# Performance work log

Hardware: AMD Instinct MI355X
Metric: run time of the kernel (lower is better)

Reference implementation:

```python
import jax, jax.numpy as jnp
import numpy as np

BLOCK_SIZE = 32
BLOCK_COUNTS = 8
N_MAX = 1024  # max seq len across jagged batch (static)
LN_EPS = 1e-5


def _silu(x):
    return x * jax.nn.sigmoid(x)


def setup_inputs() -> dict:
    key = jax.random.key(0)
    ks = jax.random.split(key, 5)
    T, H, D = 3200, 8, 128
    lengths = np.array([1024, 768, 896, 512], dtype=np.int64)
    offsets = np.concatenate([[0], np.cumsum(lengths)]).astype(np.int64)  # [B+1]
    q = jax.random.normal(ks[0], (T, H, D), jnp.float32)
    k = jax.random.normal(ks[1], (T, H, D), jnp.float32)
    v = jax.random.normal(ks[2], (T, H, D), jnp.float32)
    u = jax.random.normal(ks[3], (T, H, D), jnp.float32)
    Wg = jax.random.normal(ks[4], (H, D, 3), jnp.float32) * 0.05
    bg = jnp.zeros((H, 3), jnp.float32)
    return {"q": q, "k": k, "v": v, "u": u, "Wg": Wg, "bg": bg,
            "x_offsets": jnp.asarray(offsets)}


def _to_padded(jag, offsets, lengths, n):
    # jag: [T, H, D] -> [B, n, H, D], zero padded
    pos = jnp.arange(n)
    idx = offsets[:-1, None] + pos[None, :]                # [B, n]
    valid = pos[None, :] < lengths[:, None]                # [B, n]
    g = jag[jnp.clip(idx, 0, jag.shape[0] - 1)]            # [B, n, H, D]
    return jnp.where(valid[..., None, None], g, 0.0)


def _to_jagged(padded, offsets, T):
    tok = jnp.arange(T)
    b = jnp.searchsorted(offsets, tok, side='right') - 1   # batch id per token
    m = tok - offsets[b]                                   # local position
    return padded[b, m]


def _forward(q, k, v, u, Wg, bg, x_offsets):
    T, H, D = q.shape
    B = x_offsets.shape[0] - 1
    n = N_MAX
    bs = BLOCK_SIZE
    nb = n // bs
    S = min(BLOCK_COUNTS, nb)
    scale = D ** (-0.5)
    lengths = x_offsets[1:] - x_offsets[:-1]

    qp = _to_padded(q, x_offsets, lengths, n)  # [B, n, H, D]
    kp = _to_padded(k, x_offsets, lengths, n)
    vp = _to_padded(v, x_offsets, lengths, n)

    # gate model: per-head linear D->3 + sigmoid
    gates = jax.nn.sigmoid(jnp.einsum('bmhd,hde->bmhe', qp, Wg) + bg)
    g_cmp, g_slc = gates[..., 0], gates[..., 1]  # [B, n, H]

    # --- block compression ---
    k_cmp = kp.reshape(B, nb, bs, H, D).mean(axis=2)  # [B, nb, H, D]
    v_cmp = vp.reshape(B, nb, bs, H, D).mean(axis=2)

    # --- compressed attention + top-k block selection ---
    scores = jnp.einsum('bmhd,bkhd->bhmk', qp, k_cmp) * scale  # [B, H, n, nb]
    qblk = jnp.arange(n) // bs
    causal = qblk[:, None] >= jnp.arange(nb)[None, :]          # [n, nb]
    masked_scores = jnp.where(causal[None, None], scores, -jnp.inf)
    _, topk = jax.lax.top_k(masked_scores, S)                  # [B, H, n, S]
    topk = jnp.where(topk > qblk[None, None, :, None], -1, topk)

    p_cmp = jnp.where(causal[None, None], _silu(scores), 0.0)
    o_cmp = jnp.einsum('bhmk,bkhd->bmhd', p_cmp, v_cmp) * g_cmp[..., None]

    # --- selected (gathered top-k block) attention ---
    topk_p = jnp.transpose(topk, (0, 2, 1, 3))                 # [B, n, H, S]
    Kb = kp.reshape(B, nb, bs, H, D).transpose(0, 1, 3, 2, 4)  # [B, nb, H, bs, D]
    Vb = vp.reshape(B, nb, bs, H, D).transpose(0, 1, 3, 2, 4)
    b_ix = jnp.arange(B)[:, None, None]
    h_ix = jnp.arange(H)[None, None, :]
    m_pos = jnp.arange(n)
    off = jnp.arange(bs)

    def body(acc, s_idx):
        blk = jnp.take(topk_p, s_idx, axis=3)                  # [B, n, H]
        blk_c = jnp.maximum(blk, 0)
        Ks = Kb[b_ix, blk_c, h_ix]                             # [B, n, H, bs, D]
        Vs = Vb[b_ix, blk_c, h_ix]
        sc = jnp.einsum('bmhd,bmhkd->bmhk', qp, Ks) * scale    # [B, n, H, bs]
        kpos = blk_c[..., None] * bs + off                     # [B, n, H, bs]
        ok = (blk >= 0)[..., None] & (kpos <= m_pos[None, :, None, None])
        p = jnp.where(ok, _silu(sc), 0.0)
        acc = acc + jnp.einsum('bmhk,bmhkd->bmhd', p, Vs)
        return acc, None

    acc, _ = jax.lax.scan(jax.checkpoint(body), jnp.zeros_like(qp), jnp.arange(S))
    o_slc = acc * g_slc[..., None]

    # back to jagged, LayerNorm over flattened (H*D), gate by u
    o_cmp_j = _to_jagged(o_cmp, x_offsets, T)
    o_slc_j = _to_jagged(o_slc, x_offsets, T)

    def ln_u(x):
        xf = x.reshape(T, H * D)
        mu = xf.mean(-1, keepdims=True)
        var = ((xf - mu) ** 2).mean(-1, keepdims=True)
        xn = (xf - mu) * jax.lax.rsqrt(var + LN_EPS)
        return xn.reshape(T, H, D) * u

    out = ln_u(o_cmp_j) + ln_u(o_slc_j)
    return out, qp, kp


def reference(q, k, v, u, Wg, bg, x_offsets):
    return _forward(q, k, v, u, Wg, bg, x_offsets)
```

## Files before the change

### kernel.cpp

```cpp
#include <hip/hip_runtime.h>
#include <hip/hip_bf16.h>
#include <cmath>

#define H 8
#define D 128
#define HD 1024
#define NMAX 1024
#define BS 32
#define NB 32
#define S_SEL 8
#define CHUNK 8
#define MC 4
#define KP 136
#define NXCD 8
#define SCALE 0.08838834764831845f
#define SENT -3.0e38f

typedef __attribute__((ext_vector_type(8))) short short8;
typedef __attribute__((ext_vector_type(4))) float f32x4;

#define MFMA16(a, b, c) __builtin_amdgcn_mfma_f32_16x16x32_bf16(a, b, c, 0, 0, 0)

__device__ __forceinline__ float silu(float x) {
    return x * __builtin_amdgcn_rcpf(1.f + __expf(-x));
}
__device__ __forceinline__ float sigmoid_fast(float x) {
    return __builtin_amdgcn_rcpf(1.f + __expf(-x));
}
__device__ __forceinline__ unsigned short f2bf(float x) {
    return __builtin_bit_cast(unsigned short, __float2bfloat16(x));
}
__device__ __forceinline__ float bfup(unsigned short b) {
    unsigned u = (unsigned)b << 16;
    return __builtin_bit_cast(float, u);
}
__device__ __forceinline__ void split3(float x, unsigned short& b0,
                                       unsigned short& b1, unsigned short& b2) {
    b0 = f2bf(x);
    float r1 = x - bfup(b0);
    b1 = f2bf(r1);
    float r2 = r1 - bfup(b1);
    b2 = f2bf(r2);
}

__global__ __launch_bounds__(256) void prep_kernel(
    const float* __restrict__ q, const float* __restrict__ k,
    const float* __restrict__ v, const float* __restrict__ Wg,
    const float* __restrict__ bg, const int* __restrict__ offs,
    unsigned short* __restrict__ kb16, unsigned short* __restrict__ vt_blk,
    float* __restrict__ g, unsigned short* __restrict__ kc0,
    unsigned short* __restrict__ kc1, unsigned short* __restrict__ kc2,
    unsigned short* __restrict__ vt_cmp, float* __restrict__ o_slc,
    float* __restrict__ qp, float* __restrict__ kp) {
    int x = blockIdx.x;
    int nt = x & (NB - 1);
    int h = (x >> 5) & 7;
    int b = x >> 8;
    int o0 = offs[b];
    int len = offs[b + 1] - o0;
    int tid = threadIdx.x;
    size_t bh = (size_t)(b * H + h);
    int j = tid >> 3, dc = tid & 7;
    size_t pbase = (size_t)((b * NMAX + nt * BS + j)) * HD + h * D + dc * 16;
    if (nt * BS >= len) {
        if (tid < 128) {
            kc0[(bh * NB + nt) * 128 + tid] = 0;
            kc1[(bh * NB + nt) * 128 + tid] = 0;
            kc2[(bh * NB + nt) * 128 + tid] = 0;
            vt_cmp[(bh * 128 + tid) * NB + nt] = 0;
        }
        if (qp) {
            float4 z = make_float4(0.f, 0.f, 0.f, 0.f);
#pragma unroll
            for (int i = 0; i < 4; i++) {
                *(float4*)(qp + pbase + i * 4) = z;
                *(float4*)(kp + pbase + i * 4) = z;
            }
        }
        return;
    }

    __shared__ __align__(16) unsigned short tile[128 * 40];
    __shared__ float redK[4][128];
    __shared__ float redV[4][128];
    int w = tid >> 6, lane = tid & 63;
    size_t base = (size_t)(o0 + nt * BS + j) * HD + h * D + dc * 16;

    {
        float4 z = make_float4(0.f, 0.f, 0.f, 0.f);
#pragma unroll
        for (int i = 0; i < 4; i++) *(float4*)(o_slc + base + i * 4) = z;
    }

    {
        float xv[16];
        *(float4*)(xv + 0)  = *(const float4*)(k + base);
        *(float4*)(xv + 4)  = *(const float4*)(k + base + 4);
        *(float4*)(xv + 8)  = *(const float4*)(k + base + 8);
        *(float4*)(xv + 12) = *(const float4*)(k + base + 12);
        short8 lo, hi;
#pragma unroll
        for (int i = 0; i < 8; i++) { lo[i] = (short)f2bf(xv[i]); hi[i] = (short)f2bf(xv[8 + i]); }
        *(short8*)(kb16 + base) = lo;
        *(short8*)(kb16 + base + 8) = hi;
        if (kp) {
#pragma unroll
            for (int i = 0; i < 4; i++) *(float4*)(kp + pbase + i * 4) = *(float4*)(xv + i * 4);
        }
#pragma unroll
        for (int i = 0; i < 16; i++) {
            float s = xv[i];
            s += __shfl_xor(s, 8); s += __shfl_xor(s, 16); s += __shfl_xor(s, 32);
            if (lane < 8) redK[w][lane * 16 + i] = s;
        }
    }
    {
        float xv[16];
        *(float4*)(xv + 0)  = *(const float4*)(v + base);
        *(float4*)(xv + 4)  = *(const float4*)(v + base + 4);
        *(float4*)(xv + 8)  = *(const float4*)(v + base + 8);
        *(float4*)(xv + 12) = *(const float4*)(v + base + 12);
#pragma unroll
        for (int i = 0; i < 16; i++) tile[(dc * 16 + i) * 40 + j] = f2bf(xv[i]);
#pragma unroll
        for (int i = 0; i < 16; i++) {
            float s = xv[i];
            s += __shfl_xor(s, 8); s += __shfl_xor(s, 16); s += __shfl_xor(s, 32);
            if (lane < 8) redV[w][lane * 16 + i] = s;
        }
    }
    {
        float xv[16];
        *(float4*)(xv + 0)  = *(const float4*)(q + base);
        *(float4*)(xv + 4)  = *(const float4*)(q + base + 4);
        *(float4*)(xv + 8)  = *(const float4*)(q + base + 8);
        *(float4*)(xv + 12) = *(const float4*)(q + base + 12);
        if (qp) {
#pragma unroll
            for (int i = 0; i < 4; i++) *(float4*)(qp + pbase + i * 4) = *(float4*)(xv + i * 4);
        }
        float p0 = 0.f, p1 = 0.f;
#pragma unroll
        for (int i = 0; i < 16; i++) {
            int wb = (h * D + dc * 16 + i) * 3;
            p0 += xv[i] * Wg[wb + 0];
            p1 += xv[i] * Wg[wb + 1];
        }
#pragma unroll
        for (int off = 4; off > 0; off >>= 1) {
            p0 += __shfl_xor(p0, off);
            p1 += __shfl_xor(p1, off);
        }
        if (dc == 0) {
            float g0 = sigmoid_fast(p0 + bg[h * 3 + 0]);
            float g1 = sigmoid_fast(p1 + bg[h * 3 + 1]);
            float* gp = g + (size_t)((b * NMAX + nt * BS + j) * H + h) * 2;
            gp[0] = g0; gp[1] = g1;
        }
    }
    __syncthreads();
    {
        int d = tid >> 1, hf = tid & 1;
        short8 a = *(const short8*)(tile + d * 40 + hf * 16);
        short8 c = *(const short8*)(tile + d * 40 + hf * 16 + 8);
        size_t ob = ((bh * NB + nt) * 128 + (size_t)d) * 32 + hf * 16;
        *(short8*)(vt_blk + ob) = a;
        *(short8*)(vt_blk + ob + 8) = c;
    }
    if (tid < 128) {
        int d = tid;
        const float inv = 1.f / 32.f;
        float km = (redK[0][d] + redK[1][d] + redK[2][d] + redK[3][d]) * inv;
        float vm = (redV[0][d] + redV[1][d] + redV[2][d] + redV[3][d]) * inv;
        unsigned short e0, e1, e2;
        split3(km, e0, e1, e2);
        kc0[(bh * NB + nt) * 128 + d] = e0;
        kc1[(bh * NB + nt) * 128 + d] = e1;
        kc2[(bh * NB + nt) * 128 + d] = e2;
        vt_cmp[(bh * 128 + d) * NB + nt] = f2bf(vm);
    }
}

__global__ __launch_bounds__(256) void cmp_attn(
    const float* __restrict__ q, const unsigned short* __restrict__ kc0,
    const unsigned short* __restrict__ kc1, const unsigned short* __restrict__ kc2,
    const unsigned short* __restrict__ vt_cmp, const float* __restrict__ g,
    const int* __restrict__ offs, unsigned* __restrict__ ms_g,
    float* __restrict__ o_cmp_j) {
    int x = blockIdx.x;
    int qtile = 15 - (x & 15);
    int h = (x >> 4) & 7;
    int b = x >> 7;
    int o0 = offs[b];
    int len = offs[b + 1] - o0;
    if (qtile * 64 >= len) return;
    size_t bh = (size_t)(b * H + h);
    int qmax = 2 * qtile + 1;

    __shared__ __align__(16) unsigned short pool[3 * 4352 + 5120 + 2560];
    unsigned short* R0 = pool;
    unsigned short* R1 = pool + 4352;
    unsigned short* R2 = pool + 8704;
    unsigned short* R3 = pool + 13056;
    unsigned short* Ps = pool + 18176;

    int tid = threadIdx.x;
    int w = tid >> 6, lane = tid & 63;
    int r = lane & 15, quad = lane >> 4;
    int stg_j = tid >> 3, stg_dc = tid & 7;
    size_t msbase = (bh << 10) + (size_t)qtile * 64;

    if (stg_j <= qmax) {
        size_t src = (bh * NB + stg_j) * 128 + stg_dc * 16;
        int ofs = stg_j * 136 + stg_dc * 16;
        short8 a0 = *(const short8*)(kc0 + src);
        short8 b0 = *(const short8*)(kc0 + src + 8);
        short8 a1 = *(const short8*)(kc1 + src);
        short8 b1 = *(const short8*)(kc1 + src + 8);
        short8 a2 = *(const short8*)(kc2 + src);
        short8 b2 = *(const short8*)(kc2 + src + 8);
        *(short8*)(R0 + ofs) = a0; *(short8*)(R0 + ofs + 8) = b0;
        *(short8*)(R1 + ofs) = a1; *(short8*)(R1 + ofs + 8) = b1;
        *(short8*)(R2 + ofs) = a2; *(short8*)(R2 + ofs + 8) = b2;
    }
    {
        int d = tid >> 1, hf = tid & 1;
        short8 vv = *(const short8*)(vt_cmp + (bh * 128 + d) * NB + hf * 16);
        short8 vw = *(const short8*)(vt_cmp + (bh * 128 + d) * NB + hf * 16 + 8);
        *(short8*)(R3 + d * 40 + hf * 16) = vv;
        *(short8*)(R3 + d * 40 + hf * 16 + 8) = vw;
    }
    __syncthreads();

    short8 qf0[4], qf1[4], qf2[4];
    {
        const float* qrow = q + (size_t)(o0 + qtile * 64 + w * 16 + r) * HD + h * D;
#pragma unroll
        for (int s = 0; s < 4; s++) {
            const float* p0 = qrow + s * 32 + quad * 8;
            float xv[8];
            *(float4*)(xv) = *(const float4*)p0;
            *(float4*)(xv + 4) = *(const float4*)(p0 + 4);
            short8 f0, f1, f2;
#pragma unroll
            for (int i = 0; i < 8; i++) {
                unsigned short e0, e1, e2;
                split3(xv[i], e0, e1, e2);
                f0[i] = (short)e0; f1[i] = (short)e1; f2[i] = (short)e2;
            }
            qf0[s] = f0; qf1[s] = f1; qf2[s] = f2;
        }
    }
    auto qk6 = [&](int krow) {
        f32x4 sv = (f32x4){0.f, 0.f, 0.f, 0.f};
#pragma unroll
        for (int s = 0; s < 4; s++) {
            int ofs = krow * 136 + s * 32 + quad * 8;
            short8 k0 = *(const short8*)(R0 + ofs);
            short8 k1 = *(const short8*)(R1 + ofs);
            short8 k2 = *(const short8*)(R2 + ofs);
            sv = MFMA16(qf1[s], k1, sv);
            sv = MFMA16(qf0[s], k2, sv);
            sv = MFMA16(qf2[s], k0, sv);
            sv = MFMA16(qf0[s], k1, sv);
            sv = MFMA16(qf1[s], k0, sv);
            sv = MFMA16(qf0[s], k0, sv);
        }
        return sv;
    };
    f32x4 s0 = qk6(r);
    f32x4 s1 = (f32x4){0.f, 0.f, 0.f, 0.f};
    if (qtile >= 8) s1 = qk6(16 + r);

    float v0[4], v1[4];
#pragma unroll
    for (int jf = 0; jf < 2; jf++) {
        f32x4 svv = jf ? s1 : s0;
        int colj = jf * 16 + r;
#pragma unroll
        for (int i = 0; i < 4; i++) {
            int mrow = w * 16 + quad * 4 + i;
            int qb = 2 * qtile + (mrow >> 5);
            bool causal = (colj <= qb);
            float sc = svv[i] * SCALE;
            float val = causal ? sc : SENT;
            if (jf) v1[i] = val; else v0[i] = val;
            Ps[mrow * 40 + colj] = f2bf(causal ? silu(sc) : 0.f);
        }
    }
    if (qtile < 4) {
        if (tid < 64)
            ms_g[msbase + tid] = (1u << (2 * qtile + (tid >> 5) + 1)) - 1u;
    } else {
#pragma unroll
        for (int i = 0; i < 4; i++) {
            float a = v0[i], bb = v1[i];
            int cnt0 = (bb > a) ? 1 : 0;
            int cnt1 = (a >= bb) ? 1 : 0;
#pragma unroll
            for (int m = 1; m < 16; m++) {
                float pa = __shfl_xor(a, m);
                float pb = __shfl_xor(bb, m);
                int pc = r ^ m;
                cnt0 += ((pa > a) || (pa == a && pc < r)) ? 1 : 0;
                cnt0 += (pb > a) ? 1 : 0;
                cnt1 += ((pa > bb) || (pa == bb)) ? 1 : 0;
                cnt1 += ((pb > bb) || (pb == bb && pc < r)) ? 1 : 0;
            }
            bool sel0 = (cnt0 < S_SEL) && (a > -2.9e38f);
            bool sel1 = (cnt1 < S_SEL) && (bb > -2.9e38f);
            unsigned long long bal0 = __ballot(sel0);
            unsigned long long bal1 = __ballot(sel1);
            unsigned mask = (unsigned)((bal0 >> (16 * quad)) & 0xFFFFull)
                          | ((unsigned)((bal1 >> (16 * quad)) & 0xFFFFull) << 16);
            if (r == 0) ms_g[msbase + w * 16 + quad * 4 + i] = mask;
        }
    }
    f32x4 acc[8];
#pragma unroll
    for (int a = 0; a < 8; a++) acc[a] = (f32x4){0.f, 0.f, 0.f, 0.f};
    {
        short8 pf8 = *(const short8*)(Ps + (w * 16 + r) * 40 + quad * 8);
#pragma unroll
        for (int nf = 0; nf < 8; nf++) {
            short8 vf = *(const short8*)(R3 + (nf * 16 + r) * 40 + quad * 8);
            acc[nf] = MFMA16(pf8, vf, acc[nf]);
        }
    }
#pragma unroll
    for (int i = 0; i < 4; i++) {
        int mrow = w * 16 + quad * 4 + i;
        int gm = qtile * 64 + mrow;
        float gc = g[(size_t)((b * NMAX + gm) * H + h) * 2];
        float* dst = o_cmp_j + (size_t)(o0 + gm) * HD + h * D;
#pragma unroll
        for (int nf = 0; nf < 8; nf++)
            dst[nf * 16 + r] = acc[nf][i] * gc;
    }
}

__global__ __launch_bounds__(256) void slc_attn(
    const float* __restrict__ q, const unsigned short* __restrict__ kb16,
    const unsigned short* __restrict__ vt_blk, const float* __restrict__ g,
    const int* __restrict__ offs, const unsigned* __restrict__ ms_g,
    float* __restrict__ o_slc_j) {
    int x = blockIdx.x;
    int xcd = x & (NXCD - 1);
    int rest = x >> 3;
    int group = rest >> 6;
    int inner = rest & 63;
    int bh = group * NXCD + xcd;
    int b = bh >> 3, h = bh & 7;
    int chunk = inner & (MC - 1);
    int mtile = 15 - (inner >> 2);
    int o0 = offs[b];
    int len = offs[b + 1] - o0;
    if (mtile * 64 >= len) return;
    int qmax = 2 * mtile + 1;
    int kb0 = chunk * CHUNK;
    if (kb0 > qmax) return;
    int kend = min(qmax, kb0 + CHUNK - 1);

    __shared__ __align__(16) unsigned short pool[2 * 32 * KP + 2 * 5120 + 2560];
    __shared__ unsigned Ms[64];
    unsigned short* Kst0 = pool;
    unsigned short* Kst1 = pool + 32 * KP;
    unsigned short* Vst0 = pool + 2 * 32 * KP;
    unsigned short* Vst1 = pool + 2 * 32 * KP + 5120;
    unsigned short* Ps   = pool + 2 * 32 * KP + 10240;

    int tid = threadIdx.x;
    int w = tid >> 6, lane = tid & 63;
    int r = lane & 15, quad = lane >> 4;
    int stg_j = tid >> 3, stg_dc = tid & 7;

    if (tid < 64)
        Ms[tid] = ms_g[((size_t)bh << 10) + mtile * 64 + tid];

    short8 qs[4];
    {
        const float* qrow = q + (size_t)(o0 + mtile * 64 + w * 16 + r) * HD + h * D;
#pragma unroll
        for (int s = 0; s < 4; s++) {
            const float* p0 = qrow + s * 32 + quad * 8;
            float xv[8];
            *(float4*)(xv) = *(const float4*)p0;
            *(float4*)(xv + 4) = *(const float4*)(p0 + 4);
            short8 f;
#pragma unroll
            for (int i = 0; i < 8; i++) f[i] = (short)f2bf(xv[i]);
            qs[s] = f;
        }
    }
    f32x4 acc[8];
#pragma unroll
    for (int a = 0; a < 8; a++) acc[a] = (f32x4){0.f, 0.f, 0.f, 0.f};

    size_t vtbase = (size_t)(bh * NB) * 4096;
    int vd = tid >> 1, vhf = tid & 1;

    {
        const unsigned short* ks = kb16 + (size_t)(o0 + kb0 * BS + stg_j) * HD + h * D + stg_dc * 16;
        short8 k0 = *(const short8*)ks;
        short8 k1 = *(const short8*)(ks + 8);
        *(short8*)(Kst0 + stg_j * KP + stg_dc * 16) = k0;
        *(short8*)(Kst0 + stg_j * KP + stg_dc * 16 + 8) = k1;
        const unsigned short* vs = vt_blk + vtbase + (size_t)kb0 * 4096 + tid * 16;
        short8 v0 = *(const short8*)vs;
        short8 v1 = *(const short8*)(vs + 8);
        *(short8*)(Vst0 + vd * 40 + vhf * 16) = v0;
        *(short8*)(Vst0 + vd * 40 + vhf * 16 + 8) = v1;
    }
    __syncthreads();

    int c = 0;
    for (int kb = kb0; kb <= kend; kb++) {
        short8 pk0, pk1, pv0, pv1;
        bool pf = (kb < kend);
        if (pf) {
            const unsigned short* ks = kb16 + (size_t)(o0 + (kb + 1) * BS + stg_j) * HD + h * D + stg_dc * 16;
            pk0 = *(const short8*)ks;
            pk1 = *(const short8*)(ks + 8);
            const unsigned short* vs = vt_blk + vtbase + (size_t)(kb + 1) * 4096 + tid * 16;
            pv0 = *(const short8*)vs;
            pv1 = *(const short8*)(vs + 8);
        }
        unsigned short* K = c ? Kst1 : Kst0;
        unsigned short* V = c ? Vst1 : Vst0;
        f32x4 s0 = (f32x4){0.f, 0.f, 0.f, 0.f};
        f32x4 s1 = (f32x4){0.f, 0.f, 0.f, 0.f};
#pragma unroll
        for (int s = 0; s < 4; s++) {
            short8 kf0 = *(const short8*)(K + r * KP + s * 32 + quad * 8);
            short8 kf1 = *(const short8*)(K + (16 + r) * KP + s * 32 + quad * 8);
            s0 = MFMA16(qs[s], kf0, s0);
            s1 = MFMA16(qs[s], kf1, s1);
        }
#pragma unroll
        for (int jf = 0; jf < 2; jf++) {
            f32x4 svv = jf ? s1 : s0;
            int colj = jf * 16 + r;
            int kpos = kb * BS + colj;
#pragma unroll
            for (int i = 0; i < 4; i++) {
                int mrow = w * 16 + quad * 4 + i;
                int mpos = mtile * 64 + mrow;
                float p = (((Ms[mrow] >> kb) & 1u) && (kpos <= mpos))
                          ? silu(svv[i] * SCALE) : 0.f;
                Ps[mrow * 40 + colj] = f2bf(p);
            }
        }
        {
            short8 pf8 = *(const short8*)(Ps + (w * 16 + r) * 40 + quad * 8);
#pragma unroll
            for (int nf = 0; nf < 8; nf++) {
                short8 vf = *(const short8*)(V + (nf * 16 + r) * 40 + quad * 8);
                acc[nf] = MFMA16(pf8, vf, acc[nf]);
            }
        }
        if (pf) {
            unsigned short* Kn = c ? Kst0 : Kst1;
            unsigned short* Vn = c ? Vst0 : Vst1;
            *(short8*)(Kn + stg_j * KP + stg_dc * 16) = pk0;
            *(short8*)(Kn + stg_j * KP + stg_dc * 16 + 8) = pk1;
            *(short8*)(Vn + vd * 40 + vhf * 16) = pv0;
            *(short8*)(Vn + vd * 40 + vhf * 16 + 8) = pv1;
        }
        __syncthreads();
        c ^= 1;
    }

    bool single = (qmax < CHUNK);
#pragma unroll
    for (int i = 0; i < 4; i++) {
        int mrow = w * 16 + quad * 4 + i;
        int gm = mtile * 64 + mrow;
        float gs = g[(size_t)((b * NMAX + gm) * H + h) * 2 + 1];
        float* dst = o_slc_j + (size_t)(o0 + gm) * HD + h * D;
#pragma unroll
        for (int nf = 0; nf < 8; nf++) {
            float v0 = acc[nf][i] * gs;
            if (single) dst[nf * 16 + r] = v0;
            else        atomicAdd(dst + nf * 16 + r, v0);
        }
    }
}

__global__ __launch_bounds__(256) void pad_qk_kernel(
    const float* __restrict__ q, const float* __restrict__ k,
    const int* __restrict__ offs,
    float* __restrict__ qp, float* __restrict__ kp) {
    int idx = blockIdx.x * 256 + threadIdx.x;
    int d4 = idx & 31;
    int h  = (idx >> 5) & 7;
    int m  = (idx >> 8) & (NMAX - 1);
    int b  = idx >> 18;
    int o0 = offs[b];
    int len = offs[b + 1] - o0;
    float4 qv = make_float4(0.f, 0.f, 0.f, 0.f);
    float4 kv = qv;
    if (m < len) {
        size_t src = (size_t)(o0 + m) * HD + h * D + d4 * 4;
        qv = *(const float4*)(q + src);
        kv = *(const float4*)(k + src);
    }
    *(float4*)(qp + (size_t)idx * 4) = qv;
    *(float4*)(kp + (size_t)idx * 4) = kv;
}

__global__ __launch_bounds__(256) void ln_combine_kernel(
    const float* __restrict__ oc, const float* __restrict__ os,
    const float* __restrict__ u, float* __restrict__ out) {
    int t = blockIdx.x, tid = threadIdx.x;
    size_t base = (size_t)t * HD;
    float4 xc = *(const float4*)(oc + base + tid * 4);
    float4 xs = *(const float4*)(os + base + tid * 4);
    float4 uu = *(const float4*)(u + base + tid * 4);
    float s_c = xc.x + xc.y + xc.z + xc.w;
    float q_c = xc.x * xc.x + xc.y * xc.y + xc.z * xc.z + xc.w * xc.w;
    float s_s = xs.x + xs.y + xs.z + xs.w;
    float q_s = xs.x * xs.x + xs.y * xs.y + xs.z * xs.z + xs.w * xs.w;
#pragma unroll
    for (int off = 32; off > 0; off >>= 1) {
        s_c += __shfl_xor(s_c, off); q_c += __shfl_xor(q_c, off);
        s_s += __shfl_xor(s_s, off); q_s += __shfl_xor(q_s, off);
    }
    __shared__ float red[4][4];
    int w = tid >> 6, lane = tid & 63;
    if (lane == 0) {
        red[w][0] = s_c; red[w][1] = q_c; red[w][2] = s_s; red[w][3] = q_s;
    }
    __syncthreads();
    float tsc = red[0][0] + red[1][0] + red[2][0] + red[3][0];
    float tqc = red[0][1] + red[1][1] + red[2][1] + red[3][1];
    float tss = red[0][2] + red[1][2] + red[2][2] + red[3][2];
    float tqs = red[0][3] + red[1][3] + red[2][3] + red[3][3];
    const float inv = 1.f / 1024.f;
    float mc = tsc * inv, vc = tqc * inv - mc * mc;
    float ms = tss * inv, vs = tqs * inv - ms * ms;
    float rc = rsqrtf(vc + 1e-5f), rs = rsqrtf(vs + 1e-5f);
    float4 o;
    o.x = ((xc.x - mc) * rc + (xs.x - ms) * rs) * uu.x;
    o.y = ((xc.y - mc) * rc + (xs.y - ms) * rs) * uu.y;
    o.z = ((xc.z - mc) * rc + (xs.z - ms) * rs) * uu.z;
    o.w = ((xc.w - mc) * rc + (xs.w - ms) * rs) * uu.w;
    *(float4*)(out + base + tid * 4) = o;
}

extern "C" void kernel_launch(void* const* d_in, const int* in_sizes, int n_in,
                              void* d_out, int out_size, void* d_ws, size_t ws_size,
                              hipStream_t stream) {
    const float* q  = (const float*)d_in[0];
    const float* k  = (const float*)d_in[1];
    const float* v  = (const float*)d_in[2];
    const float* u  = (const float*)d_in[3];
    const float* Wg = (const float*)d_in[4];
    const float* bg = (const float*)d_in[5];
    const int* offs = (const int*)d_in[6];

    int B = in_sizes[6] - 1;
    int T = in_sizes[0] / HD;

    float* out = (float*)d_out;
    float* qp  = out + (size_t)T * HD;
    float* kp  = qp + (size_t)B * NMAX * HD;

    float* o_cmp_j = out;

    size_t plane = (size_t)B * H * NB * 128;
    char* w = (char*)d_ws;
    unsigned short* kc0 = (unsigned short*)w;  w += plane * 2;
    unsigned short* kc1 = (unsigned short*)w;  w += plane * 2;
    unsigned short* kc2 = (unsigned short*)w;  w += plane * 2;
    unsigned short* vt_cmp = (unsigned short*)w; w += plane * 2;
    float* g     = (float*)w;            w += (size_t)B * NMAX * H * 2 * 4;
    unsigned* ms_g = (unsigned*)w;       w += (size_t)B * H * NMAX * 4;
    float* o_slc_j = (float*)w;          w += (size_t)T * HD * 4;

    size_t kb16_bytes = (size_t)T * HD * 2;
    size_t vt_bytes   = (size_t)B * H * NB * 128 * 32 * 2;
    size_t used = (size_t)(w - (char*)d_ws);
    bool fused_pad = (used + kb16_bytes + vt_bytes <= ws_size);
    char* scr = fused_pad ? w : (char*)kp;
    unsigned short* kb16  = (unsigned short*)scr;
    unsigned short* vt_blk = (unsigned short*)(scr + kb16_bytes);

    int prepBlocks = B * H * NB;
    int cmpAttnBlocks = B * H * 16;
    int slcBlocks  = B * H * 16 * MC;
    int padBlocks  = (B * NMAX * HD / 4) / 256;

    prep_kernel<<<prepBlocks, 256, 0, stream>>>(q, k, v, Wg, bg, offs, kb16, vt_blk,
                                                g, kc0, kc1, kc2, vt_cmp, o_slc_j,
                                                fused_pad ? qp : nullptr,
                                                fused_pad ? kp : nullptr);
    cmp_attn<<<cmpAttnBlocks, 256, 0, stream>>>(q, kc0, kc1, kc2, vt_cmp, g,
                                                offs, ms_g, o_cmp_j);
    slc_attn<<<slcBlocks, 256, 0, stream>>>(q, kb16, vt_blk, g, offs, ms_g, o_slc_j);
    if (!fused_pad)
        pad_qk_kernel<<<padBlocks, 256, 0, stream>>>(q, k, offs, qp, kp);
    ln_combine_kernel<<<T, 256, 0, stream>>>(o_cmp_j, o_slc_j, u, out);
}
```

Before: 187.7 us.

## Load V fragments directly from global into registers in selected attention

The selected-block attention kernel stops staging V through double-buffered shared memory. Each lane now loads its MFMA V fragments straight from the pre-transposed global V blocks at the top of every iteration. This shrinks LDS use, and the kernel adds a launch-bounds occupancy hint of 4 blocks. The prep kernel also skips zeroing o_slc for the first 8 token tiles, which presumably are written directly rather than accumulated. The cost is unhidden global load latency for V within each iteration and higher register pressure.

```diff
diff --git a/kernel.cpp b/kernel.cpp
--- a/kernel.cpp
+++ b/kernel.cpp
@@ -86,7 +86,7 @@
     int w = tid >> 6, lane = tid & 63;
     size_t base = (size_t)(o0 + nt * BS + j) * HD + h * D + dc * 16;
 
-    {
+    if (nt >= 8) {
         float4 z = make_float4(0.f, 0.f, 0.f, 0.f);
 #pragma unroll
         for (int i = 0; i < 4; i++) *(float4*)(o_slc + base + i * 4) = z;
@@ -339,7 +339,7 @@
     }
 }
 
-__global__ __launch_bounds__(256) void slc_attn(
+__global__ __launch_bounds__(256, 4) void slc_attn(
     const float* __restrict__ q, const unsigned short* __restrict__ kb16,
     const unsigned short* __restrict__ vt_blk, const float* __restrict__ g,
     const int* __restrict__ offs, const unsigned* __restrict__ ms_g,
@@ -361,13 +361,11 @@
     if (kb0 > qmax) return;
     int kend = min(qmax, kb0 + CHUNK - 1);
 
-    __shared__ __align__(16) unsigned short pool[2 * 32 * KP + 2 * 5120 + 2560];
+    __shared__ __align__(16) unsigned short pool[2 * 32 * KP + 2560];
     __shared__ unsigned Ms[64];
     unsigned short* Kst0 = pool;
     unsigned short* Kst1 = pool + 32 * KP;
-    unsigned short* Vst0 = pool + 2 * 32 * KP;
-    unsigned short* Vst1 = pool + 2 * 32 * KP + 5120;
-    unsigned short* Ps   = pool + 2 * 32 * KP + 10240;
+    unsigned short* Ps   = pool + 2 * 32 * KP;
 
     int tid = threadIdx.x;
     int w = tid >> 6, lane = tid & 63;
@@ -397,7 +395,6 @@
     for (int a = 0; a < 8; a++) acc[a] = (f32x4){0.f, 0.f, 0.f, 0.f};
 
     size_t vtbase = (size_t)(bh * NB) * 4096;
-    int vd = tid >> 1, vhf = tid & 1;
 
     {
         const unsigned short* ks = kb16 + (size_t)(o0 + kb0 * BS + stg_j) * HD + h * D + stg_dc * 16;
@@ -405,28 +402,26 @@
         short8 k1 = *(const short8*)(ks + 8);
         *(short8*)(Kst0 + stg_j * KP + stg_dc * 16) = k0;
         *(short8*)(Kst0 + stg_j * KP + stg_dc * 16 + 8) = k1;
-        const unsigned short* vs = vt_blk + vtbase + (size_t)kb0 * 4096 + tid * 16;
-        short8 v0 = *(const short8*)vs;
-        short8 v1 = *(const short8*)(vs + 8);
-        *(short8*)(Vst0 + vd * 40 + vhf * 16) = v0;
-        *(short8*)(Vst0 + vd * 40 + vhf * 16 + 8) = v1;
     }
     __syncthreads();
 
     int c = 0;
     for (int kb = kb0; kb <= kend; kb++) {
-        short8 pk0, pk1, pv0, pv1;
+        short8 vf[8];
+        {
+            const unsigned short* vsrc = vt_blk + vtbase + (size_t)kb * 4096;
+#pragma unroll
+            for (int nf = 0; nf < 8; nf++)
+                vf[nf] = *(const short8*)(vsrc + (nf * 16 + r) * 32 + quad * 8);
+        }
+        short8 pk0, pk1;
         bool pf = (kb < kend);
         if (pf) {
             const unsigned short* ks = kb16 + (size_t)(o0 + (kb + 1) * BS + stg_j) * HD + h * D + stg_dc * 16;
             pk0 = *(const short8*)ks;
             pk1 = *(const short8*)(ks + 8);
-            const unsigned short* vs = vt_blk + vtbase + (size_t)(kb + 1) * 4096 + tid * 16;
-            pv0 = *(const short8*)vs;
-            pv1 = *(const short8*)(vs + 8);
         }
         unsigned short* K = c ? Kst1 : Kst0;
-        unsigned short* V = c ? Vst1 : Vst0;
         f32x4 s0 = (f32x4){0.f, 0.f, 0.f, 0.f};
         f32x4 s1 = (f32x4){0.f, 0.f, 0.f, 0.f};
 #pragma unroll
@@ -453,18 +448,13 @@
         {
             short8 pf8 = *(const short8*)(Ps + (w * 16 + r) * 40 + quad * 8);
 #pragma unroll
-            for (int nf = 0; nf < 8; nf++) {
-                short8 vf = *(const short8*)(V + (nf * 16 + r) * 40 + quad * 8);
-                acc[nf] = MFMA16(pf8, vf, acc[nf]);
-            }
+            for (int nf = 0; nf < 8; nf++)
+                acc[nf] = MFMA16(pf8, vf[nf], acc[nf]);
         }
         if (pf) {
             unsigned short* Kn = c ? Kst0 : Kst1;
-            unsigned short* Vn = c ? Vst0 : Vst1;
             *(short8*)(Kn + stg_j * KP + stg_dc * 16) = pk0;
             *(short8*)(Kn + stg_j * KP + stg_dc * 16 + 8) = pk1;
-            *(short8*)(Vn + vd * 40 + vhf * 16) = pv0;
-            *(short8*)(Vn + vd * 40 + vhf * 16 + 8) = pv1;
         }
         __syncthreads();
         c ^= 1;
```

Result: no change. 186.3 us (-0.8%).
